# Performance work log

Hardware: AMD Instinct MI355X
Metric: run time of the kernel (lower is better)

## Reference

```python
import jax, jax.numpy as jnp
import numpy as np

B, S, D_IN, D_OUT = 4, 2048, 4096, 4096
ACT_BITS = 8
GROUP_SIZE = 64
EPS = 1e-5


def _ste(x, q):
    # straight-through estimator: forward value q, gradient of identity
    return x + jax.lax.stop_gradient(q - x)


def absmax_quantize_dequant(x, bits=ACT_BITS, group_size=GROUP_SIZE):
    # per-token, per-group absmax fake quantization along the last dim
    qmax = float(2 ** (bits - 1) - 1)  # 127 for 8 bits
    *lead, d = x.shape
    g = group_size if group_size is not None else d
    xg = x.reshape(*lead, d // g, g)
    absmax = jnp.max(jnp.abs(xg), axis=-1, keepdims=True)
    scale = qmax / jnp.clip(absmax, EPS, None)
    q = jnp.clip(jnp.round(xg * scale), -qmax, qmax) / scale
    q = q.reshape(*lead, d)
    return _ste(x, q)


def ternary_weight_quantize_absmean(w, per_row=True):
    # BitNet b1.58: scale = mean(|W|) per output row; W_t in {-s, 0, s}
    axis = (1,) if per_row else (0, 1)
    s = jnp.mean(jnp.abs(w), axis=axis, keepdims=True)
    s = jnp.clip(s, EPS, None)
    q = jnp.clip(jnp.round(w / s), -1.0, 1.0) * s
    return _ste(w, q)


def setup_inputs() -> dict:
    key = jax.random.key(0)
    k1, k2 = jax.random.split(key)
    x = jax.random.normal(k1, (B, S, D_IN), dtype=jnp.float32)
    # kaiming-uniform-ish init scale
    bound = float(np.sqrt(1.0 / D_IN))
    weight = jax.random.uniform(k2, (D_OUT, D_IN), dtype=jnp.float32,
                                minval=-bound, maxval=bound)
    return {"x": x, "weight": weight}


def reference(x, weight):
    x_q = absmax_quantize_dequant(x)                      # [B,S,D_in]
    w_t = ternary_weight_quantize_absmean(weight)         # [D_out,D_in]
    return jnp.einsum("bsi,oi->bso", x_q, w_t)            # [B,S,D_out]
```

## Files before the change

kernel.cpp:

```cpp
#include <hip/hip_runtime.h>
#include <stdint.h>

constexpr int M = 4 * 2048;
constexpr int K = 4096;
constexpr int N = 4096;
constexpr float EPSf = 1e-5f;
constexpr float QMAX = 127.0f;

typedef __attribute__((ext_vector_type(8))) short bf16x8;
typedef __attribute__((ext_vector_type(4))) float f32x4;

__device__ __forceinline__ unsigned short f2bf(float f) {
  union { float f; uint32_t u; } c; c.f = f;
  uint32_t u = c.u;
  return (unsigned short)((u + 0x7fffu + ((u >> 16) & 1u)) >> 16);
}

__device__ __forceinline__ void async_copy16(const void* g, const void* l) {
  __builtin_amdgcn_global_load_lds(
      (const __attribute__((address_space(1))) unsigned int*)g,
      (__attribute__((address_space(3))) unsigned int*)l, 16, 0, 0);
}

__global__ void __launch_bounds__(256) quant_x_kernel(const float* __restrict__ x,
                                                      unsigned short* __restrict__ xq) {
  const int t = blockIdx.x * 256 + threadIdx.x;
  const float4 v = ((const float4*)x)[t];
  float m = fmaxf(fmaxf(fabsf(v.x), fabsf(v.y)), fmaxf(fabsf(v.z), fabsf(v.w)));
  #pragma unroll
  for (int d = 1; d < 16; d <<= 1) m = fmaxf(m, __shfl_xor(m, d));
  m = fmaxf(m, EPSf);
  const float scale = QMAX / m;

  float q0 = fminf(fmaxf(rintf(v.x * scale), -QMAX), QMAX);
  float q1 = fminf(fmaxf(rintf(v.y * scale), -QMAX), QMAX);
  float q2 = fminf(fmaxf(rintf(v.z * scale), -QMAX), QMAX);
  float q3 = fminf(fmaxf(rintf(v.w * scale), -QMAX), QMAX);
  ushort4 o;
  o.x = f2bf(q0 / scale);
  o.y = f2bf(q1 / scale);
  o.z = f2bf(q2 / scale);
  o.w = f2bf(q3 / scale);
  ((ushort4*)xq)[t] = o;
}

__global__ void __launch_bounds__(256) quant_w_kernel(const float* __restrict__ w,
                                                      unsigned short* __restrict__ wt,
                                                      float* __restrict__ wscale) {
  const int row = blockIdx.x;
  const int tid = threadIdx.x;
  const float* wr = w + (long)row * K;
  float4 v[4];
  float s = 0.f;
  #pragma unroll
  for (int p = 0; p < 4; p++) {
    v[p] = ((const float4*)wr)[tid + p * 256];
    s += fabsf(v[p].x) + fabsf(v[p].y) + fabsf(v[p].z) + fabsf(v[p].w);
  }
  #pragma unroll
  for (int d = 1; d < 64; d <<= 1) s += __shfl_xor(s, d);
  __shared__ float red[4];
  if ((tid & 63) == 0) red[tid >> 6] = s;
  __syncthreads();
  const float tot = red[0] + red[1] + red[2] + red[3];
  const float sc = fmaxf(tot / (float)K, EPSf);
  if (tid == 0) wscale[row] = sc;
  unsigned short* wrow = wt + (long)row * K;
  #pragma unroll
  for (int p = 0; p < 4; p++) {
    ushort4 o;
    o.x = f2bf(fminf(fmaxf(rintf(v[p].x / sc), -1.f), 1.f));
    o.y = f2bf(fminf(fmaxf(rintf(v[p].y / sc), -1.f), 1.f));
    o.z = f2bf(fminf(fmaxf(rintf(v[p].z / sc), -1.f), 1.f));
    o.w = f2bf(fminf(fmaxf(rintf(v[p].w / sc), -1.f), 1.f));
    ((ushort4*)wrow)[tid + p * 256] = o;
  }
}


#define BAR() do { asm volatile("" ::: "memory"); \
                   __builtin_amdgcn_s_barrier();  \
                   asm volatile("" ::: "memory"); } while (0)
#define LGKM0() asm volatile("s_waitcnt lgkmcnt(0)" ::: "memory")
#define VMCNT(n) asm volatile("s_waitcnt vmcnt(" #n ")" ::: "memory")

__global__ void __launch_bounds__(512, 2) gemm_bt_kernel(const short* __restrict__ A,
                                                         const short* __restrict__ Bt,
                                                         const float* __restrict__ wscale,
                                                         float* __restrict__ C) {
  __shared__ short smem[65536];

  const int tid  = (int)threadIdx.x;
  const int lane = tid & 63;
  const int wv   = tid >> 6;
  const int wm = wv & 1, wn = wv >> 1;
  const int quad = lane >> 4, r16 = lane & 15;

  const int f = (int)blockIdx.x;
  const int s = (f & 7) * 64 + (f >> 3);
  const int m0 = (s >> 4) * 256;
  const int n0 = (s & 15) * 256;

  const short* Ab = A  + (long)m0 * K;
  const short* Bb = Bt + (long)n0 * K;

  const int s_row8 = tid >> 3;
  const int s_kc   = ((tid & 7) ^ (s_row8 & 7)) * 8;

  const int ksw0 = (((quad * 16)      ) ^ ((r16 & 7) << 4)) >> 1;
  const int ksw1 = (((quad * 16) + 64 ) ^ ((r16 & 7) << 4)) >> 1;
  const int aro  = (wm * 64 + r16) * 64;
  const int bro  = (wn * 32 + r16) * 64;

  f32x4 acc[8][4];
  #pragma unroll
  for (int i = 0; i < 8; i++)
    #pragma unroll
    for (int j = 0; j < 4; j++) acc[i][j] = (f32x4){0.f, 0.f, 0.f, 0.f};

  bf16x8 af[4][2];
  bf16x8 bf_[2][2][2];

#define STAGE_A(buf, hh, kt) do {                                              \
    short* _d = smem + (buf) * 32768 + (hh) * 8192 + tid * 8;                  \
    const short* _g = Ab + (long)((hh) * 64 + s_row8) * K + (kt) * 64 + s_kc;  \
    async_copy16(_g, _d);                                                      \
    async_copy16(_g + (long)128 * K, _d + 4096);                               \
  } while (0)

#define STAGE_B(buf, hh, kt) do {                                              \
    short* _d = smem + (buf) * 32768 + 16384 + (hh) * 8192 + tid * 8;          \
    const int _r0 = (tid >> 8) * 64 + (hh) * 32 + (s_row8 & 31);               \
    const short* _g = Bb + (long)_r0 * K + (kt) * 64 + s_kc;                   \
    async_copy16(_g, _d);                                                      \
    async_copy16(_g + (long)128 * K, _d + 4096);                               \
  } while (0)

#define LOAD_A(buf, mi) do {                                                   \
    const short* _b = smem + (buf) * 32768 + (mi) * 8192 + aro;                \
    _Pragma("unroll") for (int _mt = 0; _mt < 4; ++_mt) {                      \
      af[_mt][0] = *(const bf16x8*)(_b + _mt * 1024 + ksw0);                   \
      af[_mt][1] = *(const bf16x8*)(_b + _mt * 1024 + ksw1);                   \
    }                                                                          \
  } while (0)

#define LOAD_B(buf, nj) do {                                                   \
    const short* _b = smem + (buf) * 32768 + 16384 + (nj) * 8192 + bro;        \
    _Pragma("unroll") for (int _nt = 0; _nt < 2; ++_nt) {                      \
      bf_[nj][_nt][0] = *(const bf16x8*)(_b + _nt * 1024 + ksw0);              \
      bf_[nj][_nt][1] = *(const bf16x8*)(_b + _nt * 1024 + ksw1);              \
    }                                                                          \
  } while (0)

#define MFMA_PHASE(mi, nj) do {                                                \
    BAR(); LGKM0();                                                            \
    __builtin_amdgcn_s_setprio(1);                                             \
    _Pragma("unroll") for (int _mt = 0; _mt < 4; ++_mt)                        \
    _Pragma("unroll") for (int _nt = 0; _nt < 2; ++_nt) {                      \
      acc[(mi)*4+_mt][(nj)*2+_nt] = __builtin_amdgcn_mfma_f32_16x16x32_bf16(   \
          af[_mt][0], bf_[nj][_nt][0], acc[(mi)*4+_mt][(nj)*2+_nt], 0, 0, 0);  \
      acc[(mi)*4+_mt][(nj)*2+_nt] = __builtin_amdgcn_mfma_f32_16x16x32_bf16(   \
          af[_mt][1], bf_[nj][_nt][1], acc[(mi)*4+_mt][(nj)*2+_nt], 0, 0, 0);  \
    }                                                                          \
    __builtin_amdgcn_s_setprio(0);                                             \
  } while (0)

  STAGE_A(0, 0, 0); STAGE_B(0, 0, 0); STAGE_B(0, 1, 0); STAGE_A(0, 1, 0);
  VMCNT(4);
  STAGE_A(1, 0, 1); STAGE_B(1, 0, 1); STAGE_B(1, 1, 1);
  VMCNT(6);
  BAR();

  for (int kt = 0; kt < 64; kt += 2) {
    const bool g2 = (kt + 2) < 64;
    const bool g3 = (kt + 3) < 64;

    LOAD_A(0, 0); LOAD_B(0, 0);
    STAGE_A(1, 1, kt + 1);
    MFMA_PHASE(0, 0); BAR();
    LOAD_B(0, 1);
    if (g2) STAGE_A(0, 0, kt + 2);
    MFMA_PHASE(0, 1); BAR();
    LOAD_A(0, 1);
    if (g2) STAGE_B(0, 0, kt + 2);
    MFMA_PHASE(1, 1); BAR();
    if (g2) STAGE_B(0, 1, kt + 2);
    MFMA_PHASE(1, 0);
    if (kt == 62) { VMCNT(0); } else { VMCNT(6); }
    BAR();

    LOAD_A(1, 0); LOAD_B(1, 0);
    if (g2) STAGE_A(0, 1, kt + 2);
    MFMA_PHASE(0, 0); BAR();
    LOAD_B(1, 1);
    if (g3) STAGE_A(1, 0, kt + 3);
    MFMA_PHASE(0, 1); BAR();
    LOAD_A(1, 1);
    if (g3) STAGE_B(1, 0, kt + 3);
    MFMA_PHASE(1, 1); BAR();
    if (g3) STAGE_B(1, 1, kt + 3);
    MFMA_PHASE(1, 0);
    if (g2) { VMCNT(6); BAR(); }
  }

  #pragma unroll
  for (int an = 0; an < 4; ++an) {
    const int col = n0 + wn * 64 + (an >> 1) * 32 + (an & 1) * 16 + r16;
    const float sc = wscale[col];
    #pragma unroll
    for (int am = 0; am < 8; ++am) {
      const int rb = m0 + wm * 128 + (am >> 2) * 64 + (am & 3) * 16 + quad * 4;
      #pragma unroll
      for (int r = 0; r < 4; ++r)
        C[(long)(rb + r) * N + col] = acc[am][an][r] * sc;
    }
  }
}

extern "C" void kernel_launch(void* const* d_in, const int* in_sizes, int n_in,
                              void* d_out, int out_size, void* d_ws, size_t ws_size,
                              hipStream_t stream) {
  const float* x   = (const float*)d_in[0];
  const float* wgt = (const float*)d_in[1];
  float* out = (float*)d_out;

  unsigned short* Aq = (unsigned short*)d_ws;
  unsigned short* Tq = Aq + (size_t)M * K;
  float* wscale = (float*)(Tq + (size_t)N * K);

  quant_x_kernel<<<(M * K / 4) / 256, 256, 0, stream>>>(x, Aq);
  quant_w_kernel<<<N, 256, 0, stream>>>(wgt, Tq, wscale);

  gemm_bt_kernel<<<dim3(512), dim3(512), 0, stream>>>((const short*)Aq, (const short*)Tq,
                                                      wscale, out);
}
```

Measured before the change: 481.2 us.

## Double-buffer MFMA fragment registers to overlap LDS reads with MFMAs

Splits the A and B register fragments into two sets (afX/afY, bS0/bS1), so LDS reads for the next quarter-tile are issued while MFMAs consume the current one. This replaces the explicit lgkmcnt(0) wait before each MFMA phase. The loop is restructured into 8 interleaved phases with a peeled epilogue, and global address offsets are precomputed as 32-bit per-thread bases. The extra live fragment registers raise register pressure under the 512x2 launch bounds, and correctness now relies on compiler-inserted LDS waits.

```diff
diff --git a/kernel.cpp b/kernel.cpp
--- a/kernel.cpp
+++ b/kernel.cpp
@@ -81,7 +81,6 @@
 #define BAR() do { asm volatile("" ::: "memory"); \
                    __builtin_amdgcn_s_barrier();  \
                    asm volatile("" ::: "memory"); } while (0)
-#define LGKM0() asm volatile("s_waitcnt lgkmcnt(0)" ::: "memory")
 #define VMCNT(n) asm volatile("s_waitcnt vmcnt(" #n ")" ::: "memory")
 
 __global__ void __launch_bounds__(512, 2) gemm_bt_kernel(const short* __restrict__ A,
@@ -106,6 +105,8 @@
 
   const int s_row8 = tid >> 3;
   const int s_kc   = ((tid & 7) ^ (s_row8 & 7)) * 8;
+  const int athr = s_row8 * K + s_kc;
+  const int bthr = ((tid >> 8) * 64 + (s_row8 & 31)) * K + s_kc;
 
   const int ksw0 = (((quad * 16)      ) ^ ((r16 & 7) << 4)) >> 1;
   const int ksw1 = (((quad * 16) + 64 ) ^ ((r16 & 7) << 4)) >> 1;
@@ -118,90 +119,92 @@
     #pragma unroll
     for (int j = 0; j < 4; j++) acc[i][j] = (f32x4){0.f, 0.f, 0.f, 0.f};
 
-  bf16x8 af[4][2];
-  bf16x8 bf_[2][2][2];
+  bf16x8 afX[4][2], afY[4][2];
+  bf16x8 bS0[2][2], bS1[2][2];
 
 #define STAGE_A(buf, hh, kt) do {                                              \
     short* _d = smem + (buf) * 32768 + (hh) * 8192 + tid * 8;                  \
-    const short* _g = Ab + (long)((hh) * 64 + s_row8) * K + (kt) * 64 + s_kc;  \
+    const short* _g = Ab + ((hh) * 64 * K + (kt) * 64) + athr;                 \
     async_copy16(_g, _d);                                                      \
-    async_copy16(_g + (long)128 * K, _d + 4096);                               \
+    async_copy16(_g + 128 * K, _d + 4096);                                     \
   } while (0)
 
 #define STAGE_B(buf, hh, kt) do {                                              \
     short* _d = smem + (buf) * 32768 + 16384 + (hh) * 8192 + tid * 8;          \
-    const int _r0 = (tid >> 8) * 64 + (hh) * 32 + (s_row8 & 31);               \
-    const short* _g = Bb + (long)_r0 * K + (kt) * 64 + s_kc;                   \
+    const short* _g = Bb + ((hh) * 32 * K + (kt) * 64) + bthr;                 \
     async_copy16(_g, _d);                                                      \
-    async_copy16(_g + (long)128 * K, _d + 4096);                               \
-  } while (0)
-
-#define LOAD_A(buf, mi) do {                                                   \
+    async_copy16(_g + 128 * K, _d + 4096);                                     \
+  } while (0)
+
+#define LOAD_A(DST, buf, mi) do {                                              \
     const short* _b = smem + (buf) * 32768 + (mi) * 8192 + aro;                \
     _Pragma("unroll") for (int _mt = 0; _mt < 4; ++_mt) {                      \
-      af[_mt][0] = *(const bf16x8*)(_b + _mt * 1024 + ksw0);                   \
-      af[_mt][1] = *(const bf16x8*)(_b + _mt * 1024 + ksw1);                   \
+      DST[_mt][0] = *(const bf16x8*)(_b + _mt * 1024 + ksw0);                  \
+      DST[_mt][1] = *(const bf16x8*)(_b + _mt * 1024 + ksw1);                  \
     }                                                                          \
   } while (0)
 
-#define LOAD_B(buf, nj) do {                                                   \
+#define LOAD_B(DST, buf, nj) do {                                              \
     const short* _b = smem + (buf) * 32768 + 16384 + (nj) * 8192 + bro;        \
     _Pragma("unroll") for (int _nt = 0; _nt < 2; ++_nt) {                      \
-      bf_[nj][_nt][0] = *(const bf16x8*)(_b + _nt * 1024 + ksw0);              \
-      bf_[nj][_nt][1] = *(const bf16x8*)(_b + _nt * 1024 + ksw1);              \
+      DST[_nt][0] = *(const bf16x8*)(_b + _nt * 1024 + ksw0);                  \
+      DST[_nt][1] = *(const bf16x8*)(_b + _nt * 1024 + ksw1);                  \
     }                                                                          \
   } while (0)
 
-#define MFMA_PHASE(mi, nj) do {                                                \
-    BAR(); LGKM0();                                                            \
+#define MFMA_Q(AF, BF, MB, NB) do {                                            \
     __builtin_amdgcn_s_setprio(1);                                             \
     _Pragma("unroll") for (int _mt = 0; _mt < 4; ++_mt)                        \
     _Pragma("unroll") for (int _nt = 0; _nt < 2; ++_nt) {                      \
-      acc[(mi)*4+_mt][(nj)*2+_nt] = __builtin_amdgcn_mfma_f32_16x16x32_bf16(   \
-          af[_mt][0], bf_[nj][_nt][0], acc[(mi)*4+_mt][(nj)*2+_nt], 0, 0, 0);  \
-      acc[(mi)*4+_mt][(nj)*2+_nt] = __builtin_amdgcn_mfma_f32_16x16x32_bf16(   \
-          af[_mt][1], bf_[nj][_nt][1], acc[(mi)*4+_mt][(nj)*2+_nt], 0, 0, 0);  \
+      acc[(MB)+_mt][(NB)+_nt] = __builtin_amdgcn_mfma_f32_16x16x32_bf16(       \
+          AF[_mt][0], BF[_nt][0], acc[(MB)+_mt][(NB)+_nt], 0, 0, 0);           \
+      acc[(MB)+_mt][(NB)+_nt] = __builtin_amdgcn_mfma_f32_16x16x32_bf16(       \
+          AF[_mt][1], BF[_nt][1], acc[(MB)+_mt][(NB)+_nt], 0, 0, 0);           \
     }                                                                          \
     __builtin_amdgcn_s_setprio(0);                                             \
   } while (0)
 
   STAGE_A(0, 0, 0); STAGE_B(0, 0, 0); STAGE_B(0, 1, 0); STAGE_A(0, 1, 0);
-  VMCNT(4);
-  STAGE_A(1, 0, 1); STAGE_B(1, 0, 1); STAGE_B(1, 1, 1);
-  VMCNT(6);
+  VMCNT(0); BAR();
+  STAGE_A(1, 0, 1); STAGE_B(1, 0, 1); STAGE_B(1, 1, 1); STAGE_A(1, 1, 1);
+  LOAD_A(afX, 0, 0); LOAD_B(bS0, 0, 0);
   BAR();
 
-  for (int kt = 0; kt < 64; kt += 2) {
-    const bool g2 = (kt + 2) < 64;
-    const bool g3 = (kt + 3) < 64;
-
-    LOAD_A(0, 0); LOAD_B(0, 0);
-    STAGE_A(1, 1, kt + 1);
-    MFMA_PHASE(0, 0); BAR();
-    LOAD_B(0, 1);
-    if (g2) STAGE_A(0, 0, kt + 2);
-    MFMA_PHASE(0, 1); BAR();
-    LOAD_A(0, 1);
-    if (g2) STAGE_B(0, 0, kt + 2);
-    MFMA_PHASE(1, 1); BAR();
-    if (g2) STAGE_B(0, 1, kt + 2);
-    MFMA_PHASE(1, 0);
-    if (kt == 62) { VMCNT(0); } else { VMCNT(6); }
-    BAR();
-
-    LOAD_A(1, 0); LOAD_B(1, 0);
-    if (g2) STAGE_A(0, 1, kt + 2);
-    MFMA_PHASE(0, 0); BAR();
-    LOAD_B(1, 1);
-    if (g3) STAGE_A(1, 0, kt + 3);
-    MFMA_PHASE(0, 1); BAR();
-    LOAD_A(1, 1);
-    if (g3) STAGE_B(1, 0, kt + 3);
-    MFMA_PHASE(1, 1); BAR();
-    if (g3) STAGE_B(1, 1, kt + 3);
-    MFMA_PHASE(1, 0);
-    if (g2) { VMCNT(6); BAR(); }
-  }
+  for (int kt = 0; kt <= 60; kt += 2) {
+    STAGE_A(0, 0, kt + 2); LOAD_B(bS1, 0, 1);
+    BAR(); MFMA_Q(afX, bS0, 0, 0); BAR();
+    STAGE_B(0, 0, kt + 2); LOAD_A(afY, 0, 1);
+    BAR(); MFMA_Q(afX, bS1, 0, 2); BAR();
+    STAGE_B(0, 1, kt + 2);
+    VMCNT(6);
+    BAR(); MFMA_Q(afY, bS1, 4, 2); BAR();
+    STAGE_A(0, 1, kt + 2); LOAD_A(afX, 1, 0); LOAD_B(bS1, 1, 0);
+    BAR(); MFMA_Q(afY, bS0, 4, 0); BAR();
+    STAGE_A(1, 0, kt + 3); LOAD_B(bS0, 1, 1);
+    BAR(); MFMA_Q(afX, bS1, 0, 0); BAR();
+    STAGE_B(1, 0, kt + 3); LOAD_A(afY, 1, 1);
+    BAR(); MFMA_Q(afX, bS0, 0, 2); BAR();
+    STAGE_B(1, 1, kt + 3);
+    VMCNT(6);
+    BAR(); MFMA_Q(afY, bS0, 4, 2); BAR();
+    STAGE_A(1, 1, kt + 3); LOAD_A(afX, 0, 0); LOAD_B(bS0, 0, 0);
+    BAR(); MFMA_Q(afY, bS1, 4, 0); BAR();
+  }
+
+  LOAD_B(bS1, 0, 1);
+  BAR(); MFMA_Q(afX, bS0, 0, 0); BAR();
+  LOAD_A(afY, 0, 1);
+  BAR(); MFMA_Q(afX, bS1, 0, 2); BAR();
+  VMCNT(0);
+  BAR(); MFMA_Q(afY, bS1, 4, 2); BAR();
+  LOAD_A(afX, 1, 0); LOAD_B(bS1, 1, 0);
+  BAR(); MFMA_Q(afY, bS0, 4, 0); BAR();
+  LOAD_B(bS0, 1, 1);
+  BAR(); MFMA_Q(afX, bS1, 0, 0); BAR();
+  LOAD_A(afY, 1, 1);
+  BAR(); MFMA_Q(afX, bS0, 0, 2); BAR();
+  BAR(); MFMA_Q(afY, bS0, 4, 2); BAR();
+  MFMA_Q(afY, bS1, 4, 0);
 
   #pragma unroll
   for (int an = 0; an < 4; ++an) {
```

Result: slower. 577.0 us (+19.9%).
